# Kernel tuning notes

Hardware: AMD Instinct MI355X
Metric: run time of the kernel (lower is better)

The kernel has to match this reference:

```python
import jax, jax.numpy as jnp
import numpy as np

N = 100000   # nodes per ntype
R = 3        # relations
E = 320000   # edges per relation
HID = 128    # hidden_dim (GATConv in_feats)
H, D = 4, 32 # num_heads, out_dim  -> H*D = 128
HD = H * D


def setup_inputs() -> dict:
    key = jax.random.key(0)
    ks = jax.random.split(key, 16)
    s = lambda k, shp, sc=0.05: jax.random.normal(k, shp, jnp.float32) * sc
    return {
        "dst_feat": s(ks[0], (N, HID), 1.0),
        "src_feats": s(ks[1], (R, N, HID), 1.0),
        "src_idx": jax.random.randint(ks[2], (R, E), 0, N, jnp.int32),
        "dst_idx": jax.random.randint(ks[3], (R, E), 0, N, jnp.int32),
        "Wt_dst": s(ks[4], (HID, HID)),
        "bt_dst": jnp.zeros((HID,), jnp.float32),
        "Wt_src": s(ks[5], (R, HID, HID)),
        "bt_src": jnp.zeros((R, HID), jnp.float32),
        "Wg": s(ks[6], (R, HID, HD)),
        "attn_l": s(ks[7], (R, H, D)),
        "attn_r": s(ks[8], (R, H, D)),
        "bias_g": jnp.zeros((R, HD), jnp.float32),
        "W1": s(ks[9], (HD, 128)),
        "b1": jnp.zeros((128,), jnp.float32),
        "W2": s(ks[10], (128, 1)),
    }


def _gat_rel(Wg, al, ar, bg, src_f, dst_f, s_idx, d_idx):
    # DGL GATConv, bipartite (src, dst), shared fc, eval mode (no dropout)
    hs = (src_f @ Wg).reshape(N, H, D)      # [N,H,D]
    hd = (dst_f @ Wg).reshape(N, H, D)
    el = (hs * al).sum(-1)                   # [N,H]
    er = (hd * ar).sum(-1)
    e = jax.nn.leaky_relu(el[s_idx] + er[d_idx], 0.2)   # [E,H]
    m = jax.ops.segment_max(e, d_idx, num_segments=N)    # edge-softmax over in-edges
    m = jnp.where(jnp.isfinite(m), m, 0.0)
    ex = jnp.exp(e - m[d_idx])
    ssum = jax.ops.segment_sum(ex, d_idx, num_segments=N)
    alpha = ex / (ssum[d_idx] + 1e-9)                    # [E,H]
    rst = jax.ops.segment_sum(alpha[:, :, None] * hs[s_idx], d_idx, num_segments=N)
    rst = rst + bg.reshape(1, H, D)
    return jax.nn.elu(rst).reshape(N, HD)


def reference(dst_feat, src_feats, src_idx, dst_idx, Wt_dst, bt_dst, Wt_src, bt_src,
              Wg, attn_l, attn_r, bias_g, W1, b1, W2):
    # weight_T per-ntype input projection (dim != hidden*num_heads branch)
    dstT = dst_feat @ Wt_dst + bt_dst                              # [N,HID]
    srcT = jnp.einsum('rnf,rfh->rnh', src_feats, Wt_src) + bt_src[:, None, :]
    # per-relation GATConv, vmapped over relations
    z_r = jax.vmap(_gat_rel, in_axes=(0, 0, 0, 0, 0, None, 0, 0))(
        Wg, attn_l, attn_r, bias_g, srcT, dstT, src_idx, dst_idx)  # [R,N,HD]
    z_m = jnp.transpose(z_r, (1, 0, 2))                            # [N,R,HD]
    # semantic attention
    w = jnp.tanh(z_m @ W1 + b1) @ W2                               # [N,R,1]
    a = jax.nn.softmax(w.mean(axis=0), axis=0)                     # [R,1]
    z = (z_m * a[None]).sum(axis=1)                                # [N,HD]
    att_mp = a.squeeze(-1)                                         # [R]
    return z, att_mp
```

## Files before the change

### kernel.cpp

```cpp
#include <hip/hip_runtime.h>
#include <hip/hip_bf16.h>
#include <math.h>

#define N_NODES 100000
#define R_REL 3
#define E_EDGES 320000
#define HID 128
#define HD 128
#define NBLK 391
#define GBLK 782

static constexpr size_t OFF_EXCSR = 0;
static constexpr size_t OFF_WTS_T = 16000000;
static constexpr size_t OFF_WG_T  = 16098304;
static constexpr size_t OFF_W1_T  = 16196608;
static constexpr size_t OFF_MER   = 16229376;
static constexpr size_t OFF_CER   = 16235520;
static constexpr size_t OFF_PART  = 16235584;
static constexpr size_t OFF_B1    = 51200000;
static constexpr size_t OFF_B2    = 204800000;
static constexpr size_t OFF_EL    = 358400000;
static constexpr size_t OFF_ER    = 363200000;
static constexpr size_t OFF_CNT   = 368006144;
static constexpr size_t OFF_OFFS  = 369206144;
static constexpr size_t OFF_CUR   = 370406272;
static constexpr size_t OFF_BSUM  = 371606272;
static constexpr size_t OFF_BOFF  = 371611136;
static constexpr size_t OFF_CSR   = 371616000;
static constexpr size_t OFF_ABUF  = 375456000;

typedef __attribute__((ext_vector_type(8))) short short8;
typedef __attribute__((ext_vector_type(4))) float floatx4;

__device__ __forceinline__ unsigned f2bf(float f)
{
    unsigned u = __float_as_uint(f);
    return (u + 0x7FFFu + ((u >> 16) & 1u)) >> 16;
}

__device__ __forceinline__ float fast_tanh(float x)
{
    x = fminf(fmaxf(x, -15.0f), 15.0f);
    float e = __expf(2.0f * x);
    return (e - 1.0f) / (e + 1.0f);
}

__global__ void transpose_bf16(const float* __restrict__ src, unsigned short* __restrict__ dst)
{
    int mat = blockIdx.y;
    int idx = blockIdx.x * 256 + threadIdx.x;
    int n = idx >> 7, k = idx & 127;
    dst[(size_t)mat * 16384 + n * 128 + k] =
        (unsigned short)f2bf(src[(size_t)mat * 16384 + k * 128 + n]);
}

__global__ __launch_bounds__(512) void prep_er(const float* __restrict__ Wg,
                                               const float* __restrict__ attn_r,
                                               const float* __restrict__ Wt_dst,
                                               const float* __restrict__ bt_dst,
                                               float* __restrict__ M, float* __restrict__ cvec)
{
    const int r = blockIdx.x;
    const int t = threadIdx.x;
    const int f = t >> 2, h = t & 3;
    __shared__ float wr[128][4];
    float s = 0.0f;
#pragma unroll
    for (int d = 0; d < 32; ++d)
        s += Wg[(size_t)r * 16384 + f * 128 + h * 32 + d] * attn_r[r * 128 + h * 32 + d];
    wr[f][h] = s;
    __syncthreads();
    float m = 0.0f;
    for (int k = 0; k < 128; ++k) m += Wt_dst[f * 128 + k] * wr[k][h];
    M[((size_t)r * 128 + f) * 4 + h] = m;
    if (f == 0) {
        float c = 0.0f;
        for (int k = 0; k < 128; ++k) c += bt_dst[k] * wr[k][h];
        cvec[r * 4 + h] = c;
    }
}

__global__ __launch_bounds__(256) void er_direct(const float* __restrict__ dst_feat,
                                                 const float* __restrict__ M,
                                                 const float* __restrict__ cvec,
                                                 float* __restrict__ er)
{
    int n = blockIdx.x * 4 + (threadIdx.x >> 6);
    int lane = threadIdx.x & 63;
    float d0 = dst_feat[(size_t)n * 128 + lane];
    float d1 = dst_feat[(size_t)n * 128 + 64 + lane];
#pragma unroll
    for (int r = 0; r < R_REL; ++r) {
        float4 w0 = *(const float4*)(M + ((size_t)r * 128 + lane) * 4);
        float4 w1 = *(const float4*)(M + ((size_t)r * 128 + 64 + lane) * 4);
        float p0 = d0 * w0.x + d1 * w1.x;
        float p1 = d0 * w0.y + d1 * w1.y;
        float p2 = d0 * w0.z + d1 * w1.z;
        float p3 = d0 * w0.w + d1 * w1.w;
#pragma unroll
        for (int off = 32; off >= 1; off >>= 1) {
            p0 += __shfl_down(p0, off);
            p1 += __shfl_down(p1, off);
            p2 += __shfl_down(p2, off);
            p3 += __shfl_down(p3, off);
        }
        if (lane == 0) {
            float4 c4 = *(const float4*)(cvec + r * 4);
            float4 o = { p0 + c4.x, p1 + c4.y, p2 + c4.z, p3 + c4.w };
            *(float4*)(er + ((size_t)r * N_NODES + n) * 4) = o;
        }
    }
}

#define XPITCH 136
__global__ __launch_bounds__(256) void fused_src_kernel(
    const float* __restrict__ src_feats, const unsigned short* __restrict__ WtsT,
    const float* __restrict__ bt_src, const unsigned short* __restrict__ WgT,
    const float* __restrict__ attn_l, float* __restrict__ hs, float* __restrict__ el)
{
    __shared__ unsigned short Xs[128 * XPITCH];
    __shared__ float els[128][4];
    const int r = blockIdx.y;
    const int row0 = blockIdx.x * 128;
    const int t = threadIdx.x, wave = t >> 6, lane = t & 63;
    const int wm = wave >> 1, wn = wave & 1, lm = lane & 15, quad = lane >> 4;
    const float* A = src_feats + (size_t)r * N_NODES * 128;

#pragma unroll
    for (int i = 0; i < 16; ++i) {
        int item = t + i * 256;
        int m = item >> 5, kq = item & 31;
        int gr = row0 + m; gr = gr < N_NODES ? gr : N_NODES - 1;
        float4 v = *(const float4*)(A + (size_t)gr * 128 + kq * 4);
        uint2 u;
        u.x = f2bf(v.x) | (f2bf(v.y) << 16);
        u.y = f2bf(v.z) | (f2bf(v.w) << 16);
        *(uint2*)(&Xs[m * XPITCH + kq * 4]) = u;
    }
    const unsigned short* B1 = WtsT + r * 16384;
    short8 bfrag[4][4];
#pragma unroll
    for (int nt = 0; nt < 4; ++nt)
#pragma unroll
        for (int kc = 0; kc < 4; ++kc)
            bfrag[nt][kc] = *(const short8*)(B1 + (wn * 64 + nt * 16 + lm) * 128 + kc * 32 + quad * 8);
    __syncthreads();

    floatx4 acc[4][4];
#pragma unroll
    for (int i = 0; i < 4; ++i)
#pragma unroll
        for (int j = 0; j < 4; ++j) acc[i][j] = (floatx4){0.f, 0.f, 0.f, 0.f};

#pragma unroll
    for (int kc = 0; kc < 4; ++kc) {
        short8 af[4];
#pragma unroll
        for (int mt = 0; mt < 4; ++mt)
            af[mt] = *(const short8*)(&Xs[(wm * 64 + mt * 16 + lm) * XPITCH + kc * 32 + quad * 8]);
#pragma unroll
        for (int mt = 0; mt < 4; ++mt)
#pragma unroll
            for (int nt = 0; nt < 4; ++nt)
                acc[mt][nt] = __builtin_amdgcn_mfma_f32_16x16x32_bf16(af[mt], bfrag[nt][kc], acc[mt][nt], 0, 0, 0);
    }
    __syncthreads();

#pragma unroll
    for (int mt = 0; mt < 4; ++mt) {
#pragma unroll
        for (int nt = 0; nt < 4; ++nt) {
            const int col = wn * 64 + nt * 16 + lm;
            const float bv = bt_src[r * 128 + col];
#pragma unroll
            for (int rg = 0; rg < 4; ++rg) {
                unsigned mb = f2bf(acc[mt][nt][rg] + bv);
                unsigned pb = (unsigned)__shfl_xor((int)mb, 1);
                if ((lm & 1) == 0) {
                    int trow = wm * 64 + mt * 16 + quad * 4 + rg;
                    *(unsigned*)(&Xs[trow * XPITCH + col]) = mb | (pb << 16);
                }
            }
        }
    }
    const unsigned short* B2 = WgT + r * 16384;
#pragma unroll
    for (int nt = 0; nt < 4; ++nt)
#pragma unroll
        for (int kc = 0; kc < 4; ++kc)
            bfrag[nt][kc] = *(const short8*)(B2 + (wn * 64 + nt * 16 + lm) * 128 + kc * 32 + quad * 8);
    __syncthreads();

#pragma unroll
    for (int i = 0; i < 4; ++i)
#pragma unroll
        for (int j = 0; j < 4; ++j) acc[i][j] = (floatx4){0.f, 0.f, 0.f, 0.f};

#pragma unroll
    for (int kc = 0; kc < 4; ++kc) {
        short8 af[4];
#pragma unroll
        for (int mt = 0; mt < 4; ++mt)
            af[mt] = *(const short8*)(&Xs[(wm * 64 + mt * 16 + lm) * XPITCH + kc * 32 + quad * 8]);
#pragma unroll
        for (int mt = 0; mt < 4; ++mt)
#pragma unroll
            for (int nt = 0; nt < 4; ++nt)
                acc[mt][nt] = __builtin_amdgcn_mfma_f32_16x16x32_bf16(af[mt], bfrag[nt][kc], acc[mt][nt], 0, 0, 0);
    }

    const float* alr = attn_l + r * 128;
    float* hsr = hs + (size_t)r * N_NODES * 128;
#pragma unroll
    for (int mt = 0; mt < 4; ++mt) {
        float eA[4] = {0.f, 0.f, 0.f, 0.f}, eB[4] = {0.f, 0.f, 0.f, 0.f};
#pragma unroll
        for (int nt = 0; nt < 4; ++nt) {
            const int col = wn * 64 + nt * 16 + lm;
            const float al = alr[col];
#pragma unroll
            for (int rg = 0; rg < 4; ++rg) {
                int gr = row0 + wm * 64 + mt * 16 + quad * 4 + rg;
                float v = acc[mt][nt][rg];
                if (gr < N_NODES) hsr[(size_t)gr * 128 + col] = v;
                float p = v * al;
                if (nt < 2) eA[rg] += p; else eB[rg] += p;
            }
        }
#pragma unroll
        for (int rg = 0; rg < 4; ++rg) {
            float a = eA[rg], b = eB[rg];
#pragma unroll
            for (int off = 8; off >= 1; off >>= 1) {
                a += __shfl_down(a, off);
                b += __shfl_down(b, off);
            }
            if (lm == 0) {
                int trow = wm * 64 + mt * 16 + quad * 4 + rg;
                els[trow][wn * 2 + 0] = a;
                els[trow][wn * 2 + 1] = b;
            }
        }
    }
    __syncthreads();
#pragma unroll
    for (int i = 0; i < 2; ++i) {
        int idx = t + i * 256;
        int trow = idx >> 2, h = idx & 3;
        int gr = row0 + trow;
        if (gr < N_NODES) el[((size_t)r * N_NODES + gr) * 4 + h] = els[trow][h];
    }
}

__global__ __launch_bounds__(256) void fused_sem_kernel(
    const float* __restrict__ zr, const unsigned short* __restrict__ W1T,
    const float* __restrict__ b1, const float* __restrict__ W2,
    float* __restrict__ partials)
{
    __shared__ unsigned short Xs[128 * XPITCH];
    const int r = blockIdx.y;
    const int row0 = blockIdx.x * 128;
    const int t = threadIdx.x, wave = t >> 6, lane = t & 63;
    const int wm = wave >> 1, wn = wave & 1, lm = lane & 15, quad = lane >> 4;
    const float* A = zr + (size_t)r * N_NODES * 128;

#pragma unroll
    for (int i = 0; i < 16; ++i) {
        int item = t + i * 256;
        int m = item >> 5, kq = item & 31;
        int gr = row0 + m; gr = gr < N_NODES ? gr : N_NODES - 1;
        float4 v = *(const float4*)(A + (size_t)gr * 128 + kq * 4);
        uint2 u;
        u.x = f2bf(v.x) | (f2bf(v.y) << 16);
        u.y = f2bf(v.z) | (f2bf(v.w) << 16);
        *(uint2*)(&Xs[m * XPITCH + kq * 4]) = u;
    }
    short8 bfrag[4][4];
#pragma unroll
    for (int nt = 0; nt < 4; ++nt)
#pragma unroll
        for (int kc = 0; kc < 4; ++kc)
            bfrag[nt][kc] = *(const short8*)(W1T + (wn * 64 + nt * 16 + lm) * 128 + kc * 32 + quad * 8);
    __syncthreads();

    floatx4 acc[4][4];
#pragma unroll
    for (int i = 0; i < 4; ++i)
#pragma unroll
        for (int j = 0; j < 4; ++j) acc[i][j] = (floatx4){0.f, 0.f, 0.f, 0.f};
#pragma unroll
    for (int kc = 0; kc < 4; ++kc) {
        short8 af[4];
#pragma unroll
        for (int mt = 0; mt < 4; ++mt)
            af[mt] = *(const short8*)(&Xs[(wm * 64 + mt * 16 + lm) * XPITCH + kc * 32 + quad * 8]);
#pragma unroll
        for (int mt = 0; mt < 4; ++mt)
#pragma unroll
            for (int nt = 0; nt < 4; ++nt)
                acc[mt][nt] = __builtin_amdgcn_mfma_f32_16x16x32_bf16(af[mt], bfrag[nt][kc], acc[mt][nt], 0, 0, 0);
    }

    float s = 0.0f;
#pragma unroll
    for (int nt = 0; nt < 4; ++nt) {
        const int col = wn * 64 + nt * 16 + lm;
        const float w2v = W2[col];
        const float b1v = b1[col];
#pragma unroll
        for (int mt = 0; mt < 4; ++mt)
#pragma unroll
            for (int rg = 0; rg < 4; ++rg) {
                int gr = row0 + wm * 64 + mt * 16 + quad * 4 + rg;
                if (gr < N_NODES) s += fast_tanh(acc[mt][nt][rg] + b1v) * w2v;
            }
    }
#pragma unroll
    for (int off = 32; off >= 1; off >>= 1) s += __shfl_down(s, off);
    __shared__ float ws4[4];
    if (lane == 0) ws4[wave] = s;
    __syncthreads();
    if (t == 0) partials[r * GBLK + blockIdx.x] = ws4[0] + ws4[1] + ws4[2] + ws4[3];
}

__global__ void count_kernel(const int* __restrict__ dst_idx, int* __restrict__ counts)
{
    int tid = blockIdx.x * 256 + threadIdx.x;
    if (tid >= R_REL * E_EDGES) return;
    int r = tid / E_EDGES;
    atomicAdd(&counts[r * N_NODES + dst_idx[tid]], 1);
}

__global__ void blocksum_kernel(const int* __restrict__ counts, int* __restrict__ bsums)
{
    int r = blockIdx.y;
    int i = blockIdx.x * 256 + threadIdx.x;
    int v = (i < N_NODES) ? counts[r * N_NODES + i] : 0;
#pragma unroll
    for (int off = 32; off >= 1; off >>= 1) v += __shfl_down(v, off);
    __shared__ int wsum[4];
    int lane = threadIdx.x & 63, w = threadIdx.x >> 6;
    if (lane == 0) wsum[w] = v;
    __syncthreads();
    if (threadIdx.x == 0) bsums[r * NBLK + blockIdx.x] = wsum[0] + wsum[1] + wsum[2] + wsum[3];
}

__global__ void scan_bsums(const int* __restrict__ bsums, int* __restrict__ boffs,
                           int* __restrict__ offs)
{
    int r = blockIdx.x;
    if (threadIdx.x != 0) return;
    int run = 0;
    for (int b = 0; b < NBLK; ++b) { boffs[r * NBLK + b] = run; run += bsums[r * NBLK + b]; }
    offs[r * (N_NODES + 1) + N_NODES] = run;
}

__global__ void scan_final(const int* __restrict__ counts, const int* __restrict__ boffs,
                           int* __restrict__ offs, int* __restrict__ cursor)
{
    int r = blockIdx.y;
    int i = blockIdx.x * 256 + threadIdx.x;
    int t = threadIdx.x;
    int v = (i < N_NODES) ? counts[r * N_NODES + i] : 0;
    __shared__ int sd[256];
    sd[t] = v;
    __syncthreads();
    for (int off = 1; off < 256; off <<= 1) {
        int y = (t >= off) ? sd[t - off] : 0;
        __syncthreads();
        sd[t] += y;
        __syncthreads();
    }
    int excl = sd[t] - v + boffs[r * NBLK + blockIdx.x];
    if (i < N_NODES) {
        offs[r * (N_NODES + 1) + i] = excl;
        cursor[r * N_NODES + i] = excl;
    }
}

__global__ void scatter_ex(const int* __restrict__ src_idx, const int* __restrict__ dst_idx,
                           const float* __restrict__ el, const float* __restrict__ er,
                           int* __restrict__ cursor, int* __restrict__ csr_src,
                           float* __restrict__ ex_csr)
{
    int tid = blockIdx.x * 256 + threadIdx.x;
    if (tid >= R_REL * E_EDGES) return;
    int r = tid / E_EDGES;
    int s = src_idx[tid], d = dst_idx[tid];
    float4 a = *(const float4*)(el + ((size_t)r * N_NODES + s) * 4);
    float4 b = *(const float4*)(er + ((size_t)r * N_NODES + d) * 4);
    float e0 = a.x + b.x, e1 = a.y + b.y, e2 = a.z + b.z, e3 = a.w + b.w;
    e0 = e0 > 0.f ? e0 : 0.2f * e0;
    e1 = e1 > 0.f ? e1 : 0.2f * e1;
    e2 = e2 > 0.f ? e2 : 0.2f * e2;
    e3 = e3 > 0.f ? e3 : 0.2f * e3;
    float4 ex = { __expf(e0), __expf(e1), __expf(e2), __expf(e3) };
    int pos = atomicAdd(&cursor[r * N_NODES + d], 1);
    csr_src[(size_t)r * E_EDGES + pos] = s;
    *(float4*)(ex_csr + ((size_t)r * E_EDGES + pos) * 4) = ex;
}

__global__ __launch_bounds__(256) void agg_kernel(
    const float* __restrict__ ex_csr, const float* __restrict__ hs,
    const int* __restrict__ offs, const int* __restrict__ csr_src,
    const float* __restrict__ bias_g, float* __restrict__ zr)
{
    int wid = blockIdx.x * 4 + (threadIdx.x >> 6);
    int r = wid / N_NODES, n = wid - r * N_NODES;
    int lane = threadIdx.x & 63;
    int h0 = lane >> 5;
    int c0 = lane, c1 = lane + 64;

    int beg = offs[r * (N_NODES + 1) + n];
    int end = offs[r * (N_NODES + 1) + n + 1];
    const int*   srcs = csr_src + (size_t)r * E_EDGES;
    const float* exc  = ex_csr + (size_t)r * E_EDGES * 4;
    const float* hsr  = hs + (size_t)r * N_NODES * HD;

    float ss0 = 0.f, ss1 = 0.f, acc0 = 0.f, acc1 = 0.f;
    for (int base = beg; base < end; base += 64) {
        int j = base + lane;
        bool v = j < end;
        int jj = v ? j : base;
        int sv = srcs[jj];
        float4 exv = *(const float4*)(exc + (size_t)jj * 4);
        if (!v) { exv.x = 0.f; exv.y = 0.f; exv.z = 0.f; exv.w = 0.f; }
        int cnt4 = (min(64, end - base) + 3) & ~3;
        for (int k = 0; k < cnt4; k += 4) {
            int s0 = __shfl(sv, k),     s1 = __shfl(sv, k + 1);
            int s2 = __shfl(sv, k + 2), s3 = __shfl(sv, k + 3);
            float x0 = __shfl(exv.x, k), y0 = __shfl(exv.y, k), z0 = __shfl(exv.z, k), w0 = __shfl(exv.w, k);
            float x1 = __shfl(exv.x, k+1), y1 = __shfl(exv.y, k+1), z1 = __shfl(exv.z, k+1), w1 = __shfl(exv.w, k+1);
            float x2 = __shfl(exv.x, k+2), y2 = __shfl(exv.y, k+2), z2 = __shfl(exv.z, k+2), w2 = __shfl(exv.w, k+2);
            float x3 = __shfl(exv.x, k+3), y3 = __shfl(exv.y, k+3), z3 = __shfl(exv.z, k+3), w3 = __shfl(exv.w, k+3);
            float g00 = hsr[(size_t)s0 * HD + c0], g01 = hsr[(size_t)s0 * HD + c1];
            float g10 = hsr[(size_t)s1 * HD + c0], g11 = hsr[(size_t)s1 * HD + c1];
            float g20 = hsr[(size_t)s2 * HD + c0], g21 = hsr[(size_t)s2 * HD + c1];
            float g30 = hsr[(size_t)s3 * HD + c0], g31 = hsr[(size_t)s3 * HD + c1];
            float e00 = h0 ? y0 : x0, e10 = h0 ? w0 : z0;
            float e01 = h0 ? y1 : x1, e11 = h0 ? w1 : z1;
            float e02 = h0 ? y2 : x2, e12 = h0 ? w2 : z2;
            float e03 = h0 ? y3 : x3, e13 = h0 ? w3 : z3;
            ss0 += e00 + e01 + e02 + e03;
            ss1 += e10 + e11 + e12 + e13;
            acc0 += e00 * g00 + e01 * g10 + e02 * g20 + e03 * g30;
            acc1 += e10 * g01 + e11 * g11 + e12 * g21 + e13 * g31;
        }
    }
    float r0 = acc0 / (ss0 + 1e-9f) + bias_g[r * HD + c0];
    float r1 = acc1 / (ss1 + 1e-9f) + bias_g[r * HD + c1];
    r0 = r0 > 0.0f ? r0 : (__expf(r0) - 1.0f);
    r1 = r1 > 0.0f ? r1 : (__expf(r1) - 1.0f);
    zr[(size_t)wid * HD + c0] = r0;
    zr[(size_t)wid * HD + c1] = r1;
}

__global__ __launch_bounds__(256) void softmax_a(const float* __restrict__ partials,
                                                 float* __restrict__ a,
                                                 float* __restrict__ out)
{
    __shared__ float sm[3];
    const int t = threadIdx.x;
    if (t < 192) {
        const int r = t >> 6, lane = t & 63;
        float v = 0.0f;
        for (int i = lane; i < GBLK; i += 64) v += partials[r * GBLK + i];
#pragma unroll
        for (int off = 32; off >= 1; off >>= 1) v += __shfl_down(v, off);
        if (lane == 0) sm[r] = v;
    }
    __syncthreads();
    if (t == 0) {
        float w0 = sm[0] / (float)N_NODES;
        float w1 = sm[1] / (float)N_NODES;
        float w2 = sm[2] / (float)N_NODES;
        float m = fmaxf(w0, fmaxf(w1, w2));
        float e0 = __expf(w0 - m), e1 = __expf(w1 - m), e2 = __expf(w2 - m);
        float s = e0 + e1 + e2;
        a[0] = e0 / s; a[1] = e1 / s; a[2] = e2 / s;
        out[(size_t)N_NODES * HD + 0] = a[0];
        out[(size_t)N_NODES * HD + 1] = a[1];
        out[(size_t)N_NODES * HD + 2] = a[2];
    }
}

__global__ __launch_bounds__(256) void combine_kernel(const float* __restrict__ zr,
                                                      const float* __restrict__ a,
                                                      float* __restrict__ out)
{
    size_t i = (size_t)blockIdx.x * 256 + threadIdx.x;
    float a0 = a[0], a1 = a[1], a2 = a[2];
    const float4 v0 = ((const float4*)zr)[i];
    const float4 v1 = ((const float4*)(zr + (size_t)N_NODES * HD))[i];
    const float4 v2 = ((const float4*)(zr + 2 * (size_t)N_NODES * HD))[i];
    float4 o = { a0 * v0.x + a1 * v1.x + a2 * v2.x,
                 a0 * v0.y + a1 * v1.y + a2 * v2.y,
                 a0 * v0.z + a1 * v1.z + a2 * v2.z,
                 a0 * v0.w + a1 * v1.w + a2 * v2.w };
    ((float4*)out)[i] = o;
}

extern "C" void kernel_launch(void* const* d_in, const int* in_sizes, int n_in,
                              void* d_out, int out_size, void* d_ws, size_t ws_size,
                              hipStream_t stream)
{
    const float* dst_feat  = (const float*)d_in[0];
    const float* src_feats = (const float*)d_in[1];
    const int*   src_idx   = (const int*)d_in[2];
    const int*   dst_idx   = (const int*)d_in[3];
    const float* Wt_dst    = (const float*)d_in[4];
    const float* bt_dst    = (const float*)d_in[5];
    const float* Wt_src    = (const float*)d_in[6];
    const float* bt_src    = (const float*)d_in[7];
    const float* Wg        = (const float*)d_in[8];
    const float* attn_l    = (const float*)d_in[9];
    const float* attn_r    = (const float*)d_in[10];
    const float* bias_g    = (const float*)d_in[11];
    const float* W1        = (const float*)d_in[12];
    const float* b1        = (const float*)d_in[13];
    const float* W2        = (const float*)d_in[14];
    float* out = (float*)d_out;

    char* ws = (char*)d_ws;
    float*          ex_csr = (float*)(ws + OFF_EXCSR);
    unsigned short* WtsT   = (unsigned short*)(ws + OFF_WTS_T);
    unsigned short* WgT    = (unsigned short*)(ws + OFF_WG_T);
    unsigned short* W1T    = (unsigned short*)(ws + OFF_W1_T);
    float*          Mer    = (float*)(ws + OFF_MER);
    float*          cer    = (float*)(ws + OFF_CER);
    float*          parts  = (float*)(ws + OFF_PART);
    float*          zr     = (float*)(ws + OFF_B1);
    float*          hs     = (float*)(ws + OFF_B2);
    float*          el     = (float*)(ws + OFF_EL);
    float*          er     = (float*)(ws + OFF_ER);
    int*            counts = (int*)(ws + OFF_CNT);
    int*            offs   = (int*)(ws + OFF_OFFS);
    int*            cursor = (int*)(ws + OFF_CUR);
    int*            bsums  = (int*)(ws + OFF_BSUM);
    int*            boffs  = (int*)(ws + OFF_BOFF);
    int*            csr    = (int*)(ws + OFF_CSR);
    float*          abuf   = (float*)(ws + OFF_ABUF);

    hipMemsetAsync(counts, 0, (size_t)R_REL * N_NODES * 4, stream);

    transpose_bf16<<<dim3(64, 3), 256, 0, stream>>>(Wt_src, WtsT);
    transpose_bf16<<<dim3(64, 3), 256, 0, stream>>>(Wg, WgT);
    transpose_bf16<<<dim3(64, 1), 256, 0, stream>>>(W1, W1T);
    prep_er<<<3, 512, 0, stream>>>(Wg, attn_r, Wt_dst, bt_dst, Mer, cer);

    fused_src_kernel<<<dim3(GBLK, 3), 256, 0, stream>>>(src_feats, WtsT, bt_src, WgT,
                                                        attn_l, hs, el);
    er_direct<<<25000, 256, 0, stream>>>(dst_feat, Mer, cer, er);

    count_kernel<<<3750, 256, 0, stream>>>(dst_idx, counts);
    blocksum_kernel<<<dim3(NBLK, 3), 256, 0, stream>>>(counts, bsums);
    scan_bsums<<<3, 64, 0, stream>>>(bsums, boffs, offs);
    scan_final<<<dim3(NBLK, 3), 256, 0, stream>>>(counts, boffs, offs, cursor);
    scatter_ex<<<3750, 256, 0, stream>>>(src_idx, dst_idx, el, er, cursor, csr, ex_csr);

    agg_kernel<<<75000, 256, 0, stream>>>(ex_csr, hs, offs, csr, bias_g, zr);

    fused_sem_kernel<<<dim3(GBLK, 3), 256, 0, stream>>>(zr, W1T, b1, W2, parts);
    softmax_a<<<1, 256, 0, stream>>>(parts, abuf, out);
    combine_kernel<<<12500, 256, 0, stream>>>(zr, abuf, out);
}
```

Before: 786.2 us.

## Loop relations inside fused src kernel with prefetch and swizzled double LDS buffers

Each block of the fused source projection kernel now processes all three relations in a loop rather than one relation per grid row. While one relation's two GEMMs run, the next relation's input rows and weights are loaded into registers, and two XOR-swizzled LDS buffers replace the padded single buffer. The el values are written straight from registers instead of through shared memory. This aims to hide global load latency and cut LDS bank conflicts, at the cost of more register pressure (launch bounds set to 2 blocks per SM) and a third as many blocks.

```diff
diff --git a/kernel.cpp b/kernel.cpp
--- a/kernel.cpp
+++ b/kernel.cpp
@@ -112,146 +112,183 @@
     }
 }
 
-#define XPITCH 136
-__global__ __launch_bounds__(256) void fused_src_kernel(
+#define SWB(row, b) (((row) << 8) | ((b) ^ (((row) & 7) << 4)))
+__global__ __launch_bounds__(256, 2) void fused_src_kernel(
     const float* __restrict__ src_feats, const unsigned short* __restrict__ WtsT,
     const float* __restrict__ bt_src, const unsigned short* __restrict__ WgT,
     const float* __restrict__ attn_l, float* __restrict__ hs, float* __restrict__ el)
 {
-    __shared__ unsigned short Xs[128 * XPITCH];
-    __shared__ float els[128][4];
-    const int r = blockIdx.y;
+    __shared__ __align__(16) unsigned short Xs[2][128 * 128];
+    char* X0 = (char*)Xs[0];
+    char* X1 = (char*)Xs[1];
     const int row0 = blockIdx.x * 128;
     const int t = threadIdx.x, wave = t >> 6, lane = t & 63;
     const int wm = wave >> 1, wn = wave & 1, lm = lane & 15, quad = lane >> 4;
-    const float* A = src_feats + (size_t)r * N_NODES * 128;
+
+    float4 L[16];
+    short8 bfrag[4][4];
 
 #pragma unroll
     for (int i = 0; i < 16; ++i) {
         int item = t + i * 256;
         int m = item >> 5, kq = item & 31;
         int gr = row0 + m; gr = gr < N_NODES ? gr : N_NODES - 1;
-        float4 v = *(const float4*)(A + (size_t)gr * 128 + kq * 4);
+        L[i] = *(const float4*)(src_feats + (size_t)gr * 128 + kq * 4);
+    }
+#pragma unroll
+    for (int nt = 0; nt < 4; ++nt)
+#pragma unroll
+        for (int kc = 0; kc < 4; ++kc)
+            bfrag[nt][kc] = *(const short8*)(WtsT + (wn * 64 + nt * 16 + lm) * 128 + kc * 32 + quad * 8);
+#pragma unroll
+    for (int i = 0; i < 16; ++i) {
+        int item = t + i * 256;
+        int m = item >> 5, kq = item & 31;
         uint2 u;
-        u.x = f2bf(v.x) | (f2bf(v.y) << 16);
-        u.y = f2bf(v.z) | (f2bf(v.w) << 16);
-        *(uint2*)(&Xs[m * XPITCH + kq * 4]) = u;
-    }
-    const unsigned short* B1 = WtsT + r * 16384;
-    short8 bfrag[4][4];
-#pragma unroll
-    for (int nt = 0; nt < 4; ++nt)
-#pragma unroll
-        for (int kc = 0; kc < 4; ++kc)
-            bfrag[nt][kc] = *(const short8*)(B1 + (wn * 64 + nt * 16 + lm) * 128 + kc * 32 + quad * 8);
-    __syncthreads();
-
-    floatx4 acc[4][4];
-#pragma unroll
-    for (int i = 0; i < 4; ++i)
-#pragma unroll
-        for (int j = 0; j < 4; ++j) acc[i][j] = (floatx4){0.f, 0.f, 0.f, 0.f};
-
-#pragma unroll
-    for (int kc = 0; kc < 4; ++kc) {
-        short8 af[4];
-#pragma unroll
-        for (int mt = 0; mt < 4; ++mt)
-            af[mt] = *(const short8*)(&Xs[(wm * 64 + mt * 16 + lm) * XPITCH + kc * 32 + quad * 8]);
-#pragma unroll
-        for (int mt = 0; mt < 4; ++mt)
-#pragma unroll
-            for (int nt = 0; nt < 4; ++nt)
-                acc[mt][nt] = __builtin_amdgcn_mfma_f32_16x16x32_bf16(af[mt], bfrag[nt][kc], acc[mt][nt], 0, 0, 0);
-    }
-    __syncthreads();
-
-#pragma unroll
-    for (int mt = 0; mt < 4; ++mt) {
-#pragma unroll
-        for (int nt = 0; nt < 4; ++nt) {
-            const int col = wn * 64 + nt * 16 + lm;
-            const float bv = bt_src[r * 128 + col];
-#pragma unroll
-            for (int rg = 0; rg < 4; ++rg) {
-                unsigned mb = f2bf(acc[mt][nt][rg] + bv);
-                unsigned pb = (unsigned)__shfl_xor((int)mb, 1);
-                if ((lm & 1) == 0) {
-                    int trow = wm * 64 + mt * 16 + quad * 4 + rg;
-                    *(unsigned*)(&Xs[trow * XPITCH + col]) = mb | (pb << 16);
+        u.x = f2bf(L[i].x) | (f2bf(L[i].y) << 16);
+        u.y = f2bf(L[i].z) | (f2bf(L[i].w) << 16);
+        *(uint2*)(X0 + SWB(m, kq * 8)) = u;
+    }
+
+    for (int r = 0; r < R_REL; ++r) {
+        __syncthreads();
+
+        if (r < R_REL - 1) {
+            const float* A = src_feats + (size_t)(r + 1) * N_NODES * 128;
+#pragma unroll
+            for (int i = 0; i < 16; ++i) {
+                int item = t + i * 256;
+                int m = item >> 5, kq = item & 31;
+                int gr = row0 + m; gr = gr < N_NODES ? gr : N_NODES - 1;
+                L[i] = *(const float4*)(A + (size_t)gr * 128 + kq * 4);
+            }
+        }
+
+        floatx4 acc[4][4];
+#pragma unroll
+        for (int i = 0; i < 4; ++i)
+#pragma unroll
+            for (int j = 0; j < 4; ++j) acc[i][j] = (floatx4){0.f, 0.f, 0.f, 0.f};
+
+#pragma unroll
+        for (int kc = 0; kc < 4; ++kc) {
+            short8 af[4];
+#pragma unroll
+            for (int mt = 0; mt < 4; ++mt)
+                af[mt] = *(const short8*)(X0 + SWB(wm * 64 + mt * 16 + lm, kc * 64 + quad * 16));
+#pragma unroll
+            for (int mt = 0; mt < 4; ++mt)
+#pragma unroll
+                for (int nt = 0; nt < 4; ++nt)
+                    acc[mt][nt] = __builtin_amdgcn_mfma_f32_16x16x32_bf16(af[mt], bfrag[nt][kc], acc[mt][nt], 0, 0, 0);
+        }
+
+#pragma unroll
+        for (int mt = 0; mt < 4; ++mt) {
+#pragma unroll
+            for (int nt = 0; nt < 4; ++nt) {
+                const int col = wn * 64 + nt * 16 + lm;
+                const float bv = bt_src[r * 128 + col];
+#pragma unroll
+                for (int rg = 0; rg < 4; ++rg) {
+                    unsigned mb = f2bf(acc[mt][nt][rg] + bv);
+                    unsigned pb = (unsigned)__shfl_xor((int)mb, 1);
+                    if ((lm & 1) == 0) {
+                        int trow = wm * 64 + mt * 16 + quad * 4 + rg;
+                        *(unsigned*)(X1 + SWB(trow, col * 2)) = mb | (pb << 16);
+                    }
                 }
             }
         }
-    }
-    const unsigned short* B2 = WgT + r * 16384;
-#pragma unroll
-    for (int nt = 0; nt < 4; ++nt)
-#pragma unroll
-        for (int kc = 0; kc < 4; ++kc)
-            bfrag[nt][kc] = *(const short8*)(B2 + (wn * 64 + nt * 16 + lm) * 128 + kc * 32 + quad * 8);
-    __syncthreads();
-
-#pragma unroll
-    for (int i = 0; i < 4; ++i)
-#pragma unroll
-        for (int j = 0; j < 4; ++j) acc[i][j] = (floatx4){0.f, 0.f, 0.f, 0.f};
-
-#pragma unroll
-    for (int kc = 0; kc < 4; ++kc) {
-        short8 af[4];
-#pragma unroll
-        for (int mt = 0; mt < 4; ++mt)
-            af[mt] = *(const short8*)(&Xs[(wm * 64 + mt * 16 + lm) * XPITCH + kc * 32 + quad * 8]);
-#pragma unroll
-        for (int mt = 0; mt < 4; ++mt)
+        {
+            const unsigned short* B2 = WgT + r * 16384;
 #pragma unroll
             for (int nt = 0; nt < 4; ++nt)
-                acc[mt][nt] = __builtin_amdgcn_mfma_f32_16x16x32_bf16(af[mt], bfrag[nt][kc], acc[mt][nt], 0, 0, 0);
-    }
-
-    const float* alr = attn_l + r * 128;
-    float* hsr = hs + (size_t)r * N_NODES * 128;
-#pragma unroll
-    for (int mt = 0; mt < 4; ++mt) {
-        float eA[4] = {0.f, 0.f, 0.f, 0.f}, eB[4] = {0.f, 0.f, 0.f, 0.f};
-#pragma unroll
-        for (int nt = 0; nt < 4; ++nt) {
-            const int col = wn * 64 + nt * 16 + lm;
-            const float al = alr[col];
+#pragma unroll
+                for (int kc = 0; kc < 4; ++kc)
+                    bfrag[nt][kc] = *(const short8*)(B2 + (wn * 64 + nt * 16 + lm) * 128 + kc * 32 + quad * 8);
+        }
+        __syncthreads();
+
+        if (r < R_REL - 1) {
+#pragma unroll
+            for (int i = 0; i < 16; ++i) {
+                int item = t + i * 256;
+                int m = item >> 5, kq = item & 31;
+                uint2 u;
+                u.x = f2bf(L[i].x) | (f2bf(L[i].y) << 16);
+                u.y = f2bf(L[i].z) | (f2bf(L[i].w) << 16);
+                *(uint2*)(X0 + SWB(m, kq * 8)) = u;
+            }
+        }
+
+#pragma unroll
+        for (int i = 0; i < 4; ++i)
+#pragma unroll
+            for (int j = 0; j < 4; ++j) acc[i][j] = (floatx4){0.f, 0.f, 0.f, 0.f};
+
+#pragma unroll
+        for (int kc = 0; kc < 4; ++kc) {
+            short8 af[4];
+#pragma unroll
+            for (int mt = 0; mt < 4; ++mt)
+                af[mt] = *(const short8*)(X1 + SWB(wm * 64 + mt * 16 + lm, kc * 64 + quad * 16));
+#pragma unroll
+            for (int mt = 0; mt < 4; ++mt)
+#pragma unroll
+                for (int nt = 0; nt < 4; ++nt)
+                    acc[mt][nt] = __builtin_amdgcn_mfma_f32_16x16x32_bf16(af[mt], bfrag[nt][kc], acc[mt][nt], 0, 0, 0);
+        }
+
+        if (r < R_REL - 1) {
+            const unsigned short* B1 = WtsT + (r + 1) * 16384;
+#pragma unroll
+            for (int nt = 0; nt < 4; ++nt)
+#pragma unroll
+                for (int kc = 0; kc < 4; ++kc)
+                    bfrag[nt][kc] = *(const short8*)(B1 + (wn * 64 + nt * 16 + lm) * 128 + kc * 32 + quad * 8);
+        }
+
+        const float* alr = attn_l + r * 128;
+        float* hsr = hs + (size_t)r * N_NODES * 128;
+        float* elr = el + (size_t)r * N_NODES * 4;
+#pragma unroll
+        for (int mt = 0; mt < 4; ++mt) {
+            float eA[4] = {0.f, 0.f, 0.f, 0.f}, eB[4] = {0.f, 0.f, 0.f, 0.f};
+#pragma unroll
+            for (int nt = 0; nt < 4; ++nt) {
+                const int col = wn * 64 + nt * 16 + lm;
+                const float al = alr[col];
+#pragma unroll
+                for (int rg = 0; rg < 4; ++rg) {
+                    int gr = row0 + wm * 64 + mt * 16 + quad * 4 + rg;
+                    float v = acc[mt][nt][rg];
+                    if (gr < N_NODES) hsr[(size_t)gr * 128 + col] = v;
+                    float p = v * al;
+                    if (nt < 2) eA[rg] += p; else eB[rg] += p;
+                }
+            }
 #pragma unroll
             for (int rg = 0; rg < 4; ++rg) {
-                int gr = row0 + wm * 64 + mt * 16 + quad * 4 + rg;
-                float v = acc[mt][nt][rg];
-                if (gr < N_NODES) hsr[(size_t)gr * 128 + col] = v;
-                float p = v * al;
-                if (nt < 2) eA[rg] += p; else eB[rg] += p;
+                float a = eA[rg], b = eB[rg];
+#pragma unroll
+                for (int off = 8; off >= 1; off >>= 1) {
+                    a += __shfl_down(a, off);
+                    b += __shfl_down(b, off);
+                }
+                if (lm == 0) {
+                    int gr = row0 + wm * 64 + mt * 16 + quad * 4 + rg;
+                    if (gr < N_NODES) {
+                        float2 o = { a, b };
+                        *(float2*)(elr + (size_t)gr * 4 + wn * 2) = o;
+                    }
+                }
             }
         }
-#pragma unroll
-        for (int rg = 0; rg < 4; ++rg) {
-            float a = eA[rg], b = eB[rg];
-#pragma unroll
-            for (int off = 8; off >= 1; off >>= 1) {
-                a += __shfl_down(a, off);
-                b += __shfl_down(b, off);
-            }
-            if (lm == 0) {
-                int trow = wm * 64 + mt * 16 + quad * 4 + rg;
-                els[trow][wn * 2 + 0] = a;
-                els[trow][wn * 2 + 1] = b;
-            }
-        }
-    }
-    __syncthreads();
-#pragma unroll
-    for (int i = 0; i < 2; ++i) {
-        int idx = t + i * 256;
-        int trow = idx >> 2, h = idx & 3;
-        int gr = row0 + trow;
-        if (gr < N_NODES) el[((size_t)r * N_NODES + gr) * 4 + h] = els[trow][h];
-    }
-}
-
+    }
+}
+
+#define XPITCH 136
 __global__ __launch_bounds__(256) void fused_sem_kernel(
     const float* __restrict__ zr, const unsigned short* __restrict__ W1T,
     const float* __restrict__ b1, const float* __restrict__ W2,
@@ -548,8 +585,8 @@
     transpose_bf16<<<dim3(64, 1), 256, 0, stream>>>(W1, W1T);
     prep_er<<<3, 512, 0, stream>>>(Wg, attn_r, Wt_dst, bt_dst, Mer, cer);
 
-    fused_src_kernel<<<dim3(GBLK, 3), 256, 0, stream>>>(src_feats, WtsT, bt_src, WgT,
-                                                        attn_l, hs, el);
+    fused_src_kernel<<<dim3(GBLK), 256, 0, stream>>>(src_feats, WtsT, bt_src, WgT,
+                                                     attn_l, hs, el);
     er_direct<<<25000, 256, 0, stream>>>(dst_feat, Mer, cer, er);
 
     count_kernel<<<3750, 256, 0, stream>>>(dst_idx, counts);
```

Result: slower. 965.3 us (+22.8%).
